# Kernel tuning notes

Measured on AMD Instinct MI355X. Metric: run time of the kernel, lower is better.

## Reference

```python
import jax, jax.numpy as jnp
import numpy as np

B, S, D = 4, 2048, 1024

def setup_inputs() -> dict:
    key = jax.random.key(0)
    k0, k1, k2, k3 = jax.random.split(key, 4)
    scale = 1.0 / np.sqrt(D)
    return {
        "x": jax.random.normal(k0, (B, S, D), dtype=jnp.float32),
        "Wq": jax.random.normal(k1, (D, D), dtype=jnp.float32) * scale,
        "Wk": jax.random.normal(k2, (D, D), dtype=jnp.float32) * scale,
        "Wv": jax.random.normal(k3, (D, D), dtype=jnp.float32) * scale,
    }

def reference(x, Wq, Wk, Wv):
    # x: [B,S,D]; Wq/Wk/Wv: [D_in, D_out] (equivalent to torch Linear weight transposed)
    q = jnp.einsum('bsd,de->bse', x, Wq)
    k = jnp.einsum('bsd,de->bse', x, Wk)
    v = jnp.einsum('bsd,de->bse', x, Wv)
    d_out = k.shape[-1]
    scores = jnp.einsum('bqe,bke->bqk', q, k)  # [B,S,S]
    S_ = scores.shape[-1]
    causal = jnp.tril(jnp.ones((S_, S_), dtype=bool))  # True = keep
    # masked_fill before scaling == after scaling (-inf invariant under positive scale)
    scores = jnp.where(causal, scores, -jnp.inf)
    attn = jax.nn.softmax(scores / jnp.sqrt(jnp.asarray(d_out, scores.dtype)), axis=-1)
    # dropout p=0.0 -> identity
    return jnp.einsum('bqk,bke->bqe', attn, v)
```

## Files before the change

### kernel.cpp

```cpp
#include <hip/hip_runtime.h>

#define B_  4
#define S_  2048
#define D_  1024
#define N_  (B_*S_)
#define SCALE 0.03125f
#define NEGINF (-3.0e38f)

typedef unsigned short u16;
typedef __attribute__((ext_vector_type(8))) short short8;
typedef __attribute__((ext_vector_type(4))) float floatx4;

__device__ __forceinline__ u16 f2bf(float f) {
    unsigned int u = __float_as_uint(f);
    u += 0x7FFFu + ((u >> 16) & 1u);
    return (u16)(u >> 16);
}
__device__ __forceinline__ float bf2f(u16 h) {
    return __uint_as_float((unsigned int)h << 16);
}

__device__ __forceinline__ void gl_lds16(const void* g, void* l) {
    __builtin_amdgcn_global_load_lds(
        (const __attribute__((address_space(1))) unsigned int*)g,
        (__attribute__((address_space(3))) unsigned int*)l, 16, 0, 0);
}

__device__ __forceinline__ int xcd_chunk(int bid, int nwg) {
    return (bid & 7) * (nwg >> 3) + (bid >> 3);
}

__global__ __launch_bounds__(256) void cast_fused(const float* __restrict__ x,
                                                  const float* __restrict__ Wq, const float* __restrict__ Wk,
                                                  const float* __restrict__ Wv,
                                                  u16* __restrict__ xb, u16* __restrict__ Wqb,
                                                  u16* __restrict__ Wkb, u16* __restrict__ Wvt) {
    __shared__ float t[32][33];
    const int blk = blockIdx.x;
    if (blk < 5120) {
        const float* src; u16* dst; size_t i;
        if (blk < 4096)      { src = x;  dst = xb;  i = (size_t)blk * 2048; }
        else if (blk < 4608) { src = Wq; dst = Wqb; i = (size_t)(blk - 4096) * 2048; }
        else                 { src = Wk; dst = Wkb; i = (size_t)(blk - 4608) * 2048; }
        i += (size_t)threadIdx.x * 8;
        float4 a = *(const float4*)&src[i];
        float4 b = *(const float4*)&src[i + 4];
        short8 o;
        o[0]=f2bf(a.x); o[1]=f2bf(a.y); o[2]=f2bf(a.z); o[3]=f2bf(a.w);
        o[4]=f2bf(b.x); o[5]=f2bf(b.y); o[6]=f2bf(b.z); o[7]=f2bf(b.w);
        *(short8*)&dst[i] = o;
    } else {
        const int tb = blk - 5120;
        const int c = threadIdx.x & 31, r0 = threadIdx.x >> 5;
        const int i0 = (tb >> 5) * 32, j0 = (tb & 31) * 32;
#pragma unroll
        for (int rr = 0; rr < 4; ++rr)
            t[r0 + rr * 8][c] = Wv[(size_t)(i0 + r0 + rr * 8) * D_ + j0 + c];
        __syncthreads();
#pragma unroll
        for (int rr = 0; rr < 4; ++rr)
            Wvt[(size_t)(j0 + r0 + rr * 8) * D_ + i0 + c] = f2bf(t[c][r0 + rr * 8]);
    }
}


__device__ __forceinline__ void mfma_nt_128(const u16* __restrict__ A, int lda,
                                            const u16* __restrict__ Bp, int ldb,
                                            int m0, int n0, int kext,
                                            u16* Sh, floatx4 acc[4][4])
{
    const int tid  = threadIdx.x;
    const int lane = tid & 63;
    const int lr   = lane & 15, quad = lane >> 4;
    const int wm   = ((tid >> 6) & 1) * 64, wn = (tid >> 7) * 64;
    const int nt   = kext >> 6;

    auto stage1 = [&](int t, int h) {
        const int kk = h >> 2, mat = (h >> 1) & 1, half = h & 1;
        const int idx = tid * 8;
        const int row = half * 64 + (idx >> 5);
        const int s   = (idx & 31) >> 3;
        const int gk  = (t << 6) + kk * 32 + ((s ^ ((row >> 1) & 3)) << 3);
        u16* dst = Sh + (t & 1) * 16384 + mat * 8192 + kk * 4096 + half * 2048 + idx;
        const u16* src = mat ? &Bp[(size_t)(n0 + row) * ldb + gk]
                             : &A [(size_t)(m0 + row) * lda + gk];
        gl_lds16(src, dst);
    };

#pragma unroll
    for (int h = 0; h < 8; ++h) stage1(0, h);

    for (int t = 0; t < nt; ++t) {
        const u16* buf = Sh + (t & 1) * 16384;
        const bool pf = (t + 1 < nt);
#pragma unroll
        for (int p = 0; p < 2; ++p) {
            if (pf) {
#pragma unroll
                for (int h = 0; h < 4; ++h) stage1(t + 1, p * 4 + h);
                asm volatile("s_waitcnt vmcnt(8)" ::: "memory");
            } else if (p == 0) {
                asm volatile("s_waitcnt vmcnt(4)" ::: "memory");
            } else {
                asm volatile("s_waitcnt vmcnt(0)" ::: "memory");
            }
            __builtin_amdgcn_s_barrier();

            short8 af[4], bf[4];
#pragma unroll
            for (int i = 0; i < 4; ++i) {
                const int ar = wm + i * 16 + lr;
                af[i] = *(const short8*)&buf[p * 4096 + ar * 32 + ((quad ^ ((ar >> 1) & 3)) << 3)];
                const int br = wn + i * 16 + lr;
                bf[i] = *(const short8*)&buf[8192 + p * 4096 + br * 32 + ((quad ^ ((br >> 1) & 3)) << 3)];
            }
            asm volatile("s_waitcnt lgkmcnt(0)" ::: "memory");
            __builtin_amdgcn_s_setprio(1);
#pragma unroll
            for (int i = 0; i < 4; ++i)
#pragma unroll
                for (int j = 0; j < 4; ++j)
                    acc[i][j] = __builtin_amdgcn_mfma_f32_16x16x32_bf16(af[i], bf[j], acc[i][j], 0, 0, 0);
            __builtin_amdgcn_s_setprio(0);
            __builtin_amdgcn_s_barrier();
        }
    }
}

#define EPI_VARS                                              \
    const int lane = threadIdx.x & 63;                        \
    const int lr = lane & 15, quad = lane >> 4;               \
    const int wm = ((threadIdx.x >> 6) & 1) * 64, wn = (threadIdx.x >> 7) * 64;

__device__ __forceinline__ void mfma_nt_256(const u16* __restrict__ A, int lda,
                                            const u16* __restrict__ Bp, int ldb,
                                            int m0, int n0, int kext,
                                            u16* Sh, floatx4 acc[8][4])
{
    const int tid  = threadIdx.x;
    const int lane = tid & 63;
    const int lr   = lane & 15, quad = lane >> 4;
    const int wr   = (tid >> 8) & 1, wc = (tid >> 6) & 3;
    const int nt   = kext >> 6;

    auto stage1 = [&](int t, int h) {
        const int kk = h >> 2, mat = (h >> 1) & 1, half = h & 1;
        const int idx = tid * 8;
        const int row = half * 128 + (idx >> 5);
        const int s   = (idx & 31) >> 3;
        const int gk  = (t << 6) + kk * 32 + ((s ^ ((row >> 1) & 3)) << 3);
        u16* dst = Sh + (t & 1) * 32768 + mat * 16384 + kk * 8192 + half * 4096 + idx;
        const u16* src = mat ? &Bp[(size_t)(n0 + row) * ldb + gk]
                             : &A [(size_t)(m0 + row) * lda + gk];
        gl_lds16(src, dst);
    };

#pragma unroll
    for (int h = 0; h < 8; ++h) stage1(0, h);

    for (int t = 0; t < nt; ++t) {
        const u16* buf = Sh + (t & 1) * 32768;
        const bool pf = (t + 1 < nt);
        short8 af[4], bf[4];

        if (pf) { stage1(t + 1, 0); stage1(t + 1, 1);
                  asm volatile("s_waitcnt vmcnt(6)" ::: "memory"); }
        else      asm volatile("s_waitcnt vmcnt(4)" ::: "memory");
        __builtin_amdgcn_s_barrier();
#pragma unroll
        for (int i = 0; i < 4; ++i) {
            const int ar = wr * 128 + i * 16 + lr;
            af[i] = *(const short8*)&buf[ar * 32 + ((quad ^ ((ar >> 1) & 3)) << 3)];
            const int br = wc * 64 + i * 16 + lr;
            bf[i] = *(const short8*)&buf[16384 + br * 32 + ((quad ^ ((br >> 1) & 3)) << 3)];
        }
        asm volatile("s_waitcnt lgkmcnt(0)" ::: "memory");
        __builtin_amdgcn_s_setprio(1);
#pragma unroll
        for (int i = 0; i < 4; ++i)
#pragma unroll
            for (int j = 0; j < 4; ++j)
                acc[i][j] = __builtin_amdgcn_mfma_f32_16x16x32_bf16(af[i], bf[j], acc[i][j], 0, 0, 0);
        __builtin_amdgcn_s_setprio(0);
        __builtin_amdgcn_s_barrier();

#pragma unroll
        for (int i = 0; i < 4; ++i) {
            const int ar = wr * 128 + 64 + i * 16 + lr;
            af[i] = *(const short8*)&buf[ar * 32 + ((quad ^ ((ar >> 1) & 3)) << 3)];
        }
        if (pf) { stage1(t + 1, 2); stage1(t + 1, 3); }
        __builtin_amdgcn_s_barrier();
        asm volatile("s_waitcnt lgkmcnt(0)" ::: "memory");
        __builtin_amdgcn_s_setprio(1);
#pragma unroll
        for (int i = 0; i < 4; ++i)
#pragma unroll
            for (int j = 0; j < 4; ++j)
                acc[4 + i][j] = __builtin_amdgcn_mfma_f32_16x16x32_bf16(af[i], bf[j], acc[4 + i][j], 0, 0, 0);
        __builtin_amdgcn_s_setprio(0);
        __builtin_amdgcn_s_barrier();

        if (pf) { stage1(t + 1, 4); stage1(t + 1, 5);
                  asm volatile("s_waitcnt vmcnt(6)" ::: "memory"); }
        else      asm volatile("s_waitcnt vmcnt(0)" ::: "memory");
        __builtin_amdgcn_s_barrier();
#pragma unroll
        for (int i = 0; i < 4; ++i) {
            const int ar = wr * 128 + i * 16 + lr;
            af[i] = *(const short8*)&buf[8192 + ar * 32 + ((quad ^ ((ar >> 1) & 3)) << 3)];
            const int br = wc * 64 + i * 16 + lr;
            bf[i] = *(const short8*)&buf[24576 + br * 32 + ((quad ^ ((br >> 1) & 3)) << 3)];
        }
        asm volatile("s_waitcnt lgkmcnt(0)" ::: "memory");
        __builtin_amdgcn_s_setprio(1);
#pragma unroll
        for (int i = 0; i < 4; ++i)
#pragma unroll
            for (int j = 0; j < 4; ++j)
                acc[i][j] = __builtin_amdgcn_mfma_f32_16x16x32_bf16(af[i], bf[j], acc[i][j], 0, 0, 0);
        __builtin_amdgcn_s_setprio(0);
        __builtin_amdgcn_s_barrier();

#pragma unroll
        for (int i = 0; i < 4; ++i) {
            const int ar = wr * 128 + 64 + i * 16 + lr;
            af[i] = *(const short8*)&buf[8192 + ar * 32 + ((quad ^ ((ar >> 1) & 3)) << 3)];
        }
        if (pf) { stage1(t + 1, 6); stage1(t + 1, 7); }
        __builtin_amdgcn_s_barrier();
        asm volatile("s_waitcnt lgkmcnt(0)" ::: "memory");
        __builtin_amdgcn_s_setprio(1);
#pragma unroll
        for (int i = 0; i < 4; ++i)
#pragma unroll
            for (int j = 0; j < 4; ++j)
                acc[4 + i][j] = __builtin_amdgcn_mfma_f32_16x16x32_bf16(af[i], bf[j], acc[4 + i][j], 0, 0, 0);
        __builtin_amdgcn_s_setprio(0);
        __builtin_amdgcn_s_barrier();
    }
}

#define EPI256_VARS                                           \
    const int lane = threadIdx.x & 63;                        \
    const int lr = lane & 15, quad = lane >> 4;               \
    const int wr = (threadIdx.x >> 8) & 1, wc = (threadIdx.x >> 6) & 3;

__global__ __launch_bounds__(256) void mt_mfma(const u16* __restrict__ Wkb, const u16* __restrict__ Wqb,
                                               u16* __restrict__ Mt)
{
    __shared__ u16 Sh[32768];
    const int m0 = blockIdx.y * 128, n0 = blockIdx.x * 128;
    floatx4 acc[4][4];
#pragma unroll
    for (int i = 0; i < 4; ++i)
#pragma unroll
        for (int j = 0; j < 4; ++j) acc[i][j] = (floatx4){0.f, 0.f, 0.f, 0.f};
    mfma_nt_128(Wkb, D_, Wqb, D_, m0, n0, D_, Sh, acc);

    EPI_VARS
#pragma unroll
    for (int i = 0; i < 4; ++i)
#pragma unroll
        for (int j = 0; j < 4; ++j)
#pragma unroll
            for (int r = 0; r < 4; ++r)
                Mt[(size_t)(m0 + wm + i * 16 + quad * 4 + r) * D_ + n0 + wn + j * 16 + lr] = f2bf(acc[i][j][r]);
}

__global__ __launch_bounds__(512, 2) void yv_mfma(const u16* __restrict__ xb, const u16* __restrict__ Mt,
                                                  const u16* __restrict__ Wvt,
                                                  u16* __restrict__ Y, u16* __restrict__ Vt)
{
    __shared__ u16 Sh[65536];
    const int lid = xcd_chunk(blockIdx.x, 256);
    floatx4 acc[8][4];
#pragma unroll
    for (int i = 0; i < 8; ++i)
#pragma unroll
        for (int j = 0; j < 4; ++j) acc[i][j] = (floatx4){0.f, 0.f, 0.f, 0.f};

    if (lid < 128) {
        const int m0 = (lid >> 2) * 256, n0 = (lid & 3) * 256;
        mfma_nt_256(xb, D_, Mt, D_, m0, n0, D_, Sh, acc);
        EPI256_VARS
#pragma unroll
        for (int i = 0; i < 8; ++i)
#pragma unroll
            for (int j = 0; j < 4; ++j)
#pragma unroll
                for (int r = 0; r < 4; ++r)
                    Y[(size_t)(m0 + wr * 128 + i * 16 + quad * 4 + r) * D_ + n0 + wc * 64 + j * 16 + lr]
                        = f2bf(acc[i][j][r]);
    } else {
        const int v = lid - 128;
        const int b = v >> 5;
        const int mloc = ((v >> 2) & 7) * 256;
        const int n0 = (v & 3) * 256;
        const int m0 = b * S_ + mloc;
        u16* Vb = Vt + (size_t)b * D_ * S_;
        mfma_nt_256(xb, D_, Wvt, D_, m0, n0, D_, Sh, acc);
        EPI256_VARS
#pragma unroll
        for (int i = 0; i < 8; ++i)
#pragma unroll
            for (int j = 0; j < 4; ++j) {
                const int ee = n0 + wc * 64 + j * 16 + lr;
                const int s4 = mloc + wr * 128 + i * 16 + quad * 4;
                ushort4 o;
                o.x = f2bf(acc[i][j][0]); o.y = f2bf(acc[i][j][1]);
                o.z = f2bf(acc[i][j][2]); o.w = f2bf(acc[i][j][3]);
                *(ushort4*)&Vb[(size_t)ee * S_ + s4] = o;
            }
    }
}

__global__ __launch_bounds__(512, 2) void scores_mfma(const u16* __restrict__ Y, const u16* __restrict__ xb,
                                                      u16* __restrict__ Sc)
{
    __shared__ u16 Sh[65536];
    const int lid = xcd_chunk(blockIdx.x, 144);
    const int b = lid / 36;
    const int t = lid - b * 36;
    int qt = 0;
    while ((qt + 1) * (qt + 2) / 2 <= t) ++qt;
    const int kt = t - qt * (qt + 1) / 2;

    const u16* A  = Y  + (size_t)b * S_ * D_;
    const u16* Bp = xb + (size_t)b * S_ * D_;
    u16* Sb = Sc + (size_t)b * S_ * S_;
    const int m0 = qt * 256, n0 = kt * 256;
    floatx4 acc[8][4];
#pragma unroll
    for (int i = 0; i < 8; ++i)
#pragma unroll
        for (int j = 0; j < 4; ++j) acc[i][j] = (floatx4){0.f, 0.f, 0.f, 0.f};
    mfma_nt_256(A, D_, Bp, D_, m0, n0, D_, Sh, acc);

    EPI256_VARS
#pragma unroll
    for (int i = 0; i < 8; ++i)
#pragma unroll
        for (int r = 0; r < 4; ++r) {
            const int grow = m0 + wr * 128 + i * 16 + quad * 4 + r;
#pragma unroll
            for (int j = 0; j < 4; ++j) {
                const int gcol = n0 + wc * 64 + j * 16 + lr;
                const float v = (gcol <= grow) ? acc[i][j][r] * SCALE : NEGINF;
                Sb[(size_t)grow * S_ + gcol] = f2bf(v);
            }
        }
}

__global__ __launch_bounds__(256) void softmax_k(const u16* __restrict__ Sc, u16* __restrict__ P)
{
    const int row = blockIdx.x;
    const int b = row >> 11, q = row & (S_ - 1);
    const int L = ((q >> 7) + 1) << 7;
    const u16* rp = Sc + ((size_t)b * S_ + q) * S_;
    u16* pp = P + ((size_t)b * S_ + q) * S_;
    __shared__ float red[4];
    __shared__ float bc;
    const int tid = threadIdx.x;
    const int i = tid << 3;
    const bool act = i < L;

    float f[8];
    float lmax = -3.4e38f;
    if (act) {
        short8 v = *(const short8*)&rp[i];
#pragma unroll
        for (int k = 0; k < 8; ++k) { f[k] = bf2f((u16)v[k]); lmax = fmaxf(lmax, f[k]); }
    }
    for (int off = 32; off; off >>= 1) lmax = fmaxf(lmax, __shfl_down(lmax, off, 64));
    if ((tid & 63) == 0) red[tid >> 6] = lmax;
    __syncthreads();
    if (tid == 0) bc = fmaxf(fmaxf(red[0], red[1]), fmaxf(red[2], red[3]));
    __syncthreads();
    const float m = bc;

    float lsum = 0.f;
    if (act) {
#pragma unroll
        for (int k = 0; k < 8; ++k) { f[k] = __expf(f[k] - m); lsum += f[k]; }
    }
    for (int off = 32; off; off >>= 1) lsum += __shfl_down(lsum, off, 64);
    if ((tid & 63) == 0) red[tid >> 6] = lsum;
    __syncthreads();
    if (tid == 0) bc = red[0] + red[1] + red[2] + red[3];
    __syncthreads();
    const float inv = 1.0f / bc;

    if (act) {
        short8 o;
#pragma unroll
        for (int k = 0; k < 8; ++k) o[k] = (short)f2bf(f[k] * inv);
        *(short8*)&pp[i] = o;
    }
}

__global__ __launch_bounds__(256) void pv_mfma(const u16* __restrict__ P, const u16* __restrict__ Vt,
                                               float* __restrict__ O)
{
    const int lid = xcd_chunk(blockIdx.x, 512);
    const int b  = lid >> 7;
    const int r  = lid & 127;
    const int et = r >> 4, qt = r & 15;
    __shared__ u16 Sh[32768];
    const u16* A  = P  + (size_t)b * S_ * S_;
    const u16* Bp = Vt + (size_t)b * D_ * S_;
    const int m0 = qt * 128, n0 = et * 128;
    const int kext = (qt + 1) * 128;
    floatx4 acc[4][4];
#pragma unroll
    for (int i = 0; i < 4; ++i)
#pragma unroll
        for (int j = 0; j < 4; ++j) acc[i][j] = (floatx4){0.f, 0.f, 0.f, 0.f};
    mfma_nt_128(A, S_, Bp, S_, m0, n0, kext, Sh, acc);

    EPI_VARS
#pragma unroll
    for (int i = 0; i < 4; ++i)
#pragma unroll
        for (int r2 = 0; r2 < 4; ++r2) {
            const int grow = m0 + wm + i * 16 + quad * 4 + r2;
#pragma unroll
            for (int j = 0; j < 4; ++j)
                O[((size_t)b * S_ + grow) * D_ + n0 + wn + j * 16 + lr] = acc[i][j][r2];
        }
}

extern "C" void kernel_launch(void* const* d_in, const int* in_sizes, int n_in,
                              void* d_out, int out_size, void* d_ws, size_t ws_size,
                              hipStream_t stream) {
    const float* x  = (const float*)d_in[0];
    const float* Wq = (const float*)d_in[1];
    const float* Wk = (const float*)d_in[2];
    const float* Wv = (const float*)d_in[3];
    float* out = (float*)d_out;
    char* w = (char*)d_ws;

    u16* xb  = (u16*)(w);
    u16* Wqb = (u16*)(w + 16777216);
    u16* Wkb = (u16*)(w + 18874368);
    u16* Wvt = (u16*)(w + 20971520);
    u16* Mt  = (u16*)(w + 23068672);
    u16* Y   = (u16*)(w + 25165824);
    u16* Vt  = (u16*)(w + 41943040);
    u16* Sc  = (u16*)(w + 58720256);
    u16* P   = (u16*)(w + 92274688);

    cast_fused <<<dim3(6144),   256, 0, stream>>>(x, Wq, Wk, Wv, xb, Wqb, Wkb, Wvt);
    mt_mfma    <<<dim3(8, 8),   256, 0, stream>>>(Wkb, Wqb, Mt);
    yv_mfma    <<<dim3(256),    512, 0, stream>>>(xb, Mt, Wvt, Y, Vt);
    scores_mfma<<<dim3(144),    512, 0, stream>>>(Y, xb, Sc);
    softmax_k  <<<dim3(N_),     256, 0, stream>>>(Sc, P);
    pv_mfma    <<<dim3(512),    256, 0, stream>>>(P, Vt, out);
}
```

Measured before the change: 226.5 us.

## Pair causal PV tiles per block and use one wave per softmax row

The PV kernel now has each 512-thread block compute two 128-row query tiles (qt and 15-qt) so causal work is balanced across blocks. It uses a new 8-wave 128x128 MFMA tile routine with 32x64 per-wave subtiles, and the grid is halved. Softmax now assigns one wavefront per row, four rows per block, and reduces with xor-shuffles only, removing the shared-memory reductions and block barriers. The cost is a second sequential K-loop per PV block and less MFMA reuse per wave.

Measured after the change: 208.4 us (median of 2 runs). 8.0% less time.

```diff
diff --git a/kernel.cpp b/kernel.cpp
--- a/kernel.cpp
+++ b/kernel.cpp
@@ -132,6 +132,73 @@
     const int lr = lane & 15, quad = lane >> 4;               \
     const int wm = ((threadIdx.x >> 6) & 1) * 64, wn = (threadIdx.x >> 7) * 64;
 
+__device__ __forceinline__ void mfma_nt_128w8(const u16* __restrict__ A, int lda,
+                                              const u16* __restrict__ Bp, int ldb,
+                                              int m0, int n0, int kext,
+                                              u16* Sh, floatx4 acc[2][4])
+{
+    const int tid  = threadIdx.x;
+    const int lane = tid & 63;
+    const int lr   = lane & 15, quad = lane >> 4;
+    const int wid  = tid >> 6;
+    const int wm   = (wid >> 1) * 32;
+    const int wn   = (wid & 1) * 64;
+    const int nt   = kext >> 6;
+
+    auto stage1 = [&](int t, int h) {
+        const int kk = h >> 1, mat = h & 1;
+        const int idx = tid * 8;
+        const int row = idx >> 5;
+        const int s   = (idx & 31) >> 3;
+        const int gk  = (t << 6) + kk * 32 + ((s ^ ((row >> 1) & 3)) << 3);
+        u16* dst = Sh + (t & 1) * 16384 + mat * 8192 + kk * 4096 + idx;
+        const u16* src = mat ? &Bp[(size_t)(n0 + row) * ldb + gk]
+                             : &A [(size_t)(m0 + row) * lda + gk];
+        gl_lds16(src, dst);
+    };
+
+#pragma unroll
+    for (int h = 0; h < 4; ++h) stage1(0, h);
+
+    for (int t = 0; t < nt; ++t) {
+        const u16* buf = Sh + (t & 1) * 16384;
+        const bool pf = (t + 1 < nt);
+#pragma unroll
+        for (int p = 0; p < 2; ++p) {
+            if (pf) {
+                stage1(t + 1, p * 2); stage1(t + 1, p * 2 + 1);
+                asm volatile("s_waitcnt vmcnt(4)" ::: "memory");
+            } else if (p == 0) {
+                asm volatile("s_waitcnt vmcnt(2)" ::: "memory");
+            } else {
+                asm volatile("s_waitcnt vmcnt(0)" ::: "memory");
+            }
+            __builtin_amdgcn_s_barrier();
+
+            short8 af[2], bf[4];
+#pragma unroll
+            for (int i = 0; i < 2; ++i) {
+                const int ar = wm + i * 16 + lr;
+                af[i] = *(const short8*)&buf[p * 4096 + ar * 32 + ((quad ^ ((ar >> 1) & 3)) << 3)];
+            }
+#pragma unroll
+            for (int j = 0; j < 4; ++j) {
+                const int br = wn + j * 16 + lr;
+                bf[j] = *(const short8*)&buf[8192 + p * 4096 + br * 32 + ((quad ^ ((br >> 1) & 3)) << 3)];
+            }
+            asm volatile("s_waitcnt lgkmcnt(0)" ::: "memory");
+            __builtin_amdgcn_s_setprio(1);
+#pragma unroll
+            for (int i = 0; i < 2; ++i)
+#pragma unroll
+                for (int j = 0; j < 4; ++j)
+                    acc[i][j] = __builtin_amdgcn_mfma_f32_16x16x32_bf16(af[i], bf[j], acc[i][j], 0, 0, 0);
+            __builtin_amdgcn_s_setprio(0);
+            __builtin_amdgcn_s_barrier();
+        }
+    }
+}
+
 __device__ __forceinline__ void mfma_nt_256(const u16* __restrict__ A, int lda,
                                             const u16* __restrict__ Bp, int ldb,
                                             int m0, int n0, int kext,
@@ -354,80 +421,97 @@
 
 __global__ __launch_bounds__(256) void softmax_k(const u16* __restrict__ Sc, u16* __restrict__ P)
 {
-    const int row = blockIdx.x;
+    const int row = blockIdx.x * 4 + (threadIdx.x >> 6);
+    const int lane = threadIdx.x & 63;
     const int b = row >> 11, q = row & (S_ - 1);
     const int L = ((q >> 7) + 1) << 7;
     const u16* rp = Sc + ((size_t)b * S_ + q) * S_;
     u16* pp = P + ((size_t)b * S_ + q) * S_;
-    __shared__ float red[4];
-    __shared__ float bc;
-    const int tid = threadIdx.x;
-    const int i = tid << 3;
-    const bool act = i < L;
-
-    float f[8];
+
+    float f[4][8];
     float lmax = -3.4e38f;
-    if (act) {
-        short8 v = *(const short8*)&rp[i];
-#pragma unroll
-        for (int k = 0; k < 8; ++k) { f[k] = bf2f((u16)v[k]); lmax = fmaxf(lmax, f[k]); }
-    }
-    for (int off = 32; off; off >>= 1) lmax = fmaxf(lmax, __shfl_down(lmax, off, 64));
-    if ((tid & 63) == 0) red[tid >> 6] = lmax;
-    __syncthreads();
-    if (tid == 0) bc = fmaxf(fmaxf(red[0], red[1]), fmaxf(red[2], red[3]));
-    __syncthreads();
-    const float m = bc;
+#pragma unroll
+    for (int c = 0; c < 4; ++c) {
+        const int i = c * 512 + lane * 8;
+        if (i < L) {
+            short8 v = *(const short8*)&rp[i];
+#pragma unroll
+            for (int k = 0; k < 8; ++k) { f[c][k] = bf2f((u16)v[k]); lmax = fmaxf(lmax, f[c][k]); }
+        }
+    }
+#pragma unroll
+    for (int off = 32; off; off >>= 1) lmax = fmaxf(lmax, __shfl_xor(lmax, off, 64));
 
     float lsum = 0.f;
-    if (act) {
-#pragma unroll
-        for (int k = 0; k < 8; ++k) { f[k] = __expf(f[k] - m); lsum += f[k]; }
-    }
-    for (int off = 32; off; off >>= 1) lsum += __shfl_down(lsum, off, 64);
-    if ((tid & 63) == 0) red[tid >> 6] = lsum;
-    __syncthreads();
-    if (tid == 0) bc = red[0] + red[1] + red[2] + red[3];
-    __syncthreads();
-    const float inv = 1.0f / bc;
-
-    if (act) {
-        short8 o;
-#pragma unroll
-        for (int k = 0; k < 8; ++k) o[k] = (short)f2bf(f[k] * inv);
-        *(short8*)&pp[i] = o;
-    }
-}
-
-__global__ __launch_bounds__(256) void pv_mfma(const u16* __restrict__ P, const u16* __restrict__ Vt,
-                                               float* __restrict__ O)
-{
-    const int lid = xcd_chunk(blockIdx.x, 512);
-    const int b  = lid >> 7;
-    const int r  = lid & 127;
-    const int et = r >> 4, qt = r & 15;
+#pragma unroll
+    for (int c = 0; c < 4; ++c) {
+        const int i = c * 512 + lane * 8;
+        if (i < L) {
+#pragma unroll
+            for (int k = 0; k < 8; ++k) { f[c][k] = __expf(f[c][k] - lmax); lsum += f[c][k]; }
+        }
+    }
+#pragma unroll
+    for (int off = 32; off; off >>= 1) lsum += __shfl_xor(lsum, off, 64);
+    const float inv = 1.0f / lsum;
+
+#pragma unroll
+    for (int c = 0; c < 4; ++c) {
+        const int i = c * 512 + lane * 8;
+        if (i < L) {
+            short8 o;
+#pragma unroll
+            for (int k = 0; k < 8; ++k) o[k] = (short)f2bf(f[c][k] * inv);
+            *(short8*)&pp[i] = o;
+        }
+    }
+}
+
+__device__ __forceinline__ void pv_epi(floatx4 acc[2][4], int b, int m0, int n0, float* __restrict__ O)
+{
+    const int lane = threadIdx.x & 63;
+    const int lr = lane & 15, quad = lane >> 4;
+    const int wid = threadIdx.x >> 6;
+    const int wm = (wid >> 1) * 32, wn = (wid & 1) * 64;
+#pragma unroll
+    for (int i = 0; i < 2; ++i)
+#pragma unroll
+        for (int r = 0; r < 4; ++r) {
+            const int grow = m0 + wm + i * 16 + quad * 4 + r;
+#pragma unroll
+            for (int j = 0; j < 4; ++j)
+                O[((size_t)b * S_ + grow) * D_ + n0 + wn + j * 16 + lr] = acc[i][j][r];
+        }
+}
+
+__global__ __launch_bounds__(512, 2) void pv_mfma(const u16* __restrict__ P, const u16* __restrict__ Vt,
+                                                  float* __restrict__ O)
+{
     __shared__ u16 Sh[32768];
+    const int lid = xcd_chunk(blockIdx.x, 256);
+    const int b  = lid >> 6;
+    const int et = (lid >> 3) & 7;
+    const int pr = lid & 7;
+    const int n0 = et * 128;
     const u16* A  = P  + (size_t)b * S_ * S_;
     const u16* Bp = Vt + (size_t)b * D_ * S_;
-    const int m0 = qt * 128, n0 = et * 128;
-    const int kext = (qt + 1) * 128;
-    floatx4 acc[4][4];
-#pragma unroll
-    for (int i = 0; i < 4; ++i)
+
+    floatx4 acc[2][4];
+    const int qtA = pr, qtB = 15 - pr;
+
+#pragma unroll
+    for (int i = 0; i < 2; ++i)
 #pragma unroll
         for (int j = 0; j < 4; ++j) acc[i][j] = (floatx4){0.f, 0.f, 0.f, 0.f};
-    mfma_nt_128(A, S_, Bp, S_, m0, n0, kext, Sh, acc);
-
-    EPI_VARS
-#pragma unroll
-    for (int i = 0; i < 4; ++i)
-#pragma unroll
-        for (int r2 = 0; r2 < 4; ++r2) {
-            const int grow = m0 + wm + i * 16 + quad * 4 + r2;
-#pragma unroll
-            for (int j = 0; j < 4; ++j)
-                O[((size_t)b * S_ + grow) * D_ + n0 + wn + j * 16 + lr] = acc[i][j][r2];
-        }
+    mfma_nt_128w8(A, S_, Bp, S_, qtA * 128, n0, (qtA + 1) * 128, Sh, acc);
+    pv_epi(acc, b, qtA * 128, n0, O);
+
+#pragma unroll
+    for (int i = 0; i < 2; ++i)
+#pragma unroll
+        for (int j = 0; j < 4; ++j) acc[i][j] = (floatx4){0.f, 0.f, 0.f, 0.f};
+    mfma_nt_128w8(A, S_, Bp, S_, qtB * 128, n0, (qtB + 1) * 128, Sh, acc);
+    pv_epi(acc, b, qtB * 128, n0, O);
 }
 
 extern "C" void kernel_launch(void* const* d_in, const int* in_sizes, int n_in,
@@ -454,6 +538,6 @@
     mt_mfma    <<<dim3(8, 8),   256, 0, stream>>>(Wkb, Wqb, Mt);
     yv_mfma    <<<dim3(256),    512, 0, stream>>>(xb, Mt, Wvt, Y, Vt);
     scores_mfma<<<dim3(144),    512, 0, stream>>>(Y, xb, Sc);
-    softmax_k  <<<dim3(N_),     256, 0, stream>>>(Sc, P);
-    pv_mfma    <<<dim3(512),    256, 0, stream>>>(P, Vt, out);
-}
+    softmax_k  <<<dim3(N_/4),   256, 0, stream>>>(Sc, P);
+    pv_mfma    <<<dim3(256),    512, 0, stream>>>(P, Vt, out);
+}
```
